# Kernel optimization log

Hardware: AMD Instinct MI355X
Metric: run time of the kernel (lower is better)

The kernel has to match this reference:

```python
import jax, jax.numpy as jnp
from jax import lax
import numpy as np

B = 4096          # batch
EMBED = 32        # embed_dim
HEADS = 2
MEM_SIZE = 4096
MEM_DIM = 256
TOPK = 10
LN_EPS = 1e-5


def setup_inputs() -> dict:
    key = jax.random.key(0)
    ks = jax.random.split(key, 32)
    rn = lambda i, shape, s=0.05: (jax.random.normal(ks[i], shape) * s).astype(jnp.float32)
    return {
        'x': jax.random.normal(ks[0], (B, 1, 28, 28), dtype=jnp.float32),
        'patch_w': rn(1, (32, 1, 4, 4)), 'patch_b': rn(2, (32,)),
        'blk_ln1_g': jnp.ones((2, 32), jnp.float32), 'blk_ln1_b': jnp.zeros((2, 32), jnp.float32),
        'blk_inproj_w': rn(3, (2, 96, 32)), 'blk_inproj_b': rn(4, (2, 96)),
        'blk_outproj_w': rn(5, (2, 32, 32)), 'blk_outproj_b': rn(6, (2, 32)),
        'blk_ln2_g': jnp.ones((2, 32), jnp.float32), 'blk_ln2_b': jnp.zeros((2, 32), jnp.float32),
        'blk_ff1_w': rn(7, (2, 128, 32)), 'blk_ff1_b': rn(8, (2, 128)),
        'blk_ff2_w': rn(9, (2, 32, 128)), 'blk_ff2_b': rn(10, (2, 32)),
        'lat_w': rn(11, (256, 1568)), 'lat_b': rn(12, (256,)),
        'memory': jax.random.normal(ks[13], (MEM_SIZE, MEM_DIM), dtype=jnp.float32),
        'dec_w': rn(14, (3136, 256)), 'dec_b': rn(15, (3136,)),
        'upt1_w': rn(16, (64, 32, 4, 4)), 'upt1_b': rn(17, (32,)),
        'c1_w': rn(18, (32, 32, 3, 3)), 'c1_b': rn(19, (32,)),
        'upt2_w': rn(20, (32, 16, 4, 4)), 'upt2_b': rn(21, (16,)),
        'c2_w': rn(22, (8, 16, 3, 3)), 'c2_b': rn(23, (8,)),
        'c3_w': rn(24, (1, 8, 1, 1)), 'c3_b': rn(25, (1,)),
    }


def _ln(x, g, b):
    m = jnp.mean(x, -1, keepdims=True)
    v = jnp.mean((x - m) ** 2, -1, keepdims=True)
    return (x - m) / jnp.sqrt(v + LN_EPS) * g + b


def _conv2d(x, w, b, stride=1, pad=0):
    out = lax.conv_general_dilated(x, w, (stride, stride), ((pad, pad), (pad, pad)),
                                   dimension_numbers=('NCHW', 'OIHW', 'NCHW'))
    return out + b[None, :, None, None]


def _conv_transpose2d(x, w, b, stride, pad):
    # w in torch layout [in, out, kh, kw]; equivalent fractionally-strided conv
    w_f = jnp.flip(w, (2, 3)).transpose(1, 0, 2, 3)  # OIHW
    k = w.shape[2]
    p = k - 1 - pad
    out = lax.conv_general_dilated(x, w_f, (1, 1), ((p, p), (p, p)),
                                   lhs_dilation=(stride, stride),
                                   dimension_numbers=('NCHW', 'OIHW', 'NCHW'))
    return out + b[None, :, None, None]


def _mha(x, wi, bi, wo, bo):
    Bn, S, D = x.shape
    Dh = D // HEADS
    qkv = x @ wi.T + bi                                  # [B,S,3D]
    q, k, v = jnp.split(qkv, 3, axis=-1)
    sp = lambda t: t.reshape(Bn, S, HEADS, Dh).transpose(0, 2, 1, 3)
    q, k, v = sp(q), sp(k), sp(v)
    scores = jnp.einsum('bhqd,bhkd->bhqk', q, k) / jnp.sqrt(jnp.asarray(Dh, x.dtype))
    att = jax.nn.softmax(scores, axis=-1)
    o = jnp.einsum('bhqk,bhkd->bhqd', att, v).transpose(0, 2, 1, 3).reshape(Bn, S, D)
    return o @ wo.T + bo


def _memory_read(latent, memory):
    # cosine-sim topk softmax-weighted gather (F.normalize eps=1e-12)
    mn = memory / jnp.clip(jnp.linalg.norm(memory, axis=1, keepdims=True), 1e-12)
    xn = latent / jnp.clip(jnp.linalg.norm(latent, axis=1, keepdims=True), 1e-12)
    sim = xn @ mn.T                                       # [B, MEM_SIZE]
    topk_sim, topk_idx = lax.top_k(sim, TOPK)
    w = jax.nn.softmax(topk_sim, axis=1)                  # [B, TOPK]
    sel = memory[topk_idx]                                # [B, TOPK, MEM_DIM]
    return jnp.einsum('bk,bkd->bd', w, sel)


def _forward(x, patch_w, patch_b, blk_ln1_g, blk_ln1_b, blk_inproj_w, blk_inproj_b,
             blk_outproj_w, blk_outproj_b, blk_ln2_g, blk_ln2_b, blk_ff1_w, blk_ff1_b,
             blk_ff2_w, blk_ff2_b, lat_w, lat_b, memory, dec_w, dec_b,
             upt1_w, upt1_b, c1_w, c1_b, upt2_w, upt2_b, c2_w, c2_b, c3_w, c3_b):
    Bn = x.shape[0]
    h = _conv2d(x, patch_w, patch_b, stride=4)            # [B,32,7,7]
    t = h.reshape(Bn, EMBED, 49).transpose(0, 2, 1)       # [B,49,32]
    for i in range(2):                                    # two SwinBlocks
        t = t + _mha(_ln(t, blk_ln1_g[i], blk_ln1_b[i]),
                     blk_inproj_w[i], blk_inproj_b[i], blk_outproj_w[i], blk_outproj_b[i])
        f = _ln(t, blk_ln2_g[i], blk_ln2_b[i])
        f = jax.nn.gelu(f @ blk_ff1_w[i].T + blk_ff1_b[i], approximate=False)
        t = t + (f @ blk_ff2_w[i].T + blk_ff2_b[i])
    latent = t.reshape(Bn, -1) @ lat_w.T + lat_b          # [B,256]
    mem_latent = _memory_read(latent, memory)             # [B,256]
    d = (mem_latent @ dec_w.T + dec_b).reshape(Bn, 64, 7, 7)  # dropout=eval identity
    d = jax.nn.relu(_conv_transpose2d(d, upt1_w, upt1_b, 2, 1))   # [B,32,14,14]
    d = jax.nn.relu(_conv2d(d, c1_w, c1_b, 1, 1))
    d = jax.nn.relu(_conv_transpose2d(d, upt2_w, upt2_b, 2, 1))   # [B,16,28,28]
    d = jax.nn.relu(_conv2d(d, c2_w, c2_b, 1, 1))                 # [B,8,28,28]
    return _conv2d(d, c3_w, c3_b, 1, 0)                           # [B,1,28,28]


def reference(x, patch_w, patch_b, blk_ln1_g, blk_ln1_b, blk_inproj_w, blk_inproj_b,
              blk_outproj_w, blk_outproj_b, blk_ln2_g, blk_ln2_b, blk_ff1_w, blk_ff1_b,
              blk_ff2_w, blk_ff2_b, lat_w, lat_b, memory, dec_w, dec_b,
              upt1_w, upt1_b, c1_w, c1_b, upt2_w, upt2_b, c2_w, c2_b, c3_w, c3_b):
    return _forward(x, patch_w, patch_b, blk_ln1_g, blk_ln1_b, blk_inproj_w, blk_inproj_b,
                    blk_outproj_w, blk_outproj_b, blk_ln2_g, blk_ln2_b, blk_ff1_w, blk_ff1_b,
                    blk_ff2_w, blk_ff2_b, lat_w, lat_b, memory, dec_w, dec_b,
                    upt1_w, upt1_b, c1_w, c1_b, upt2_w, upt2_b, c2_w, c2_b, c3_w, c3_b)
```

## Files before the change

### kernel.cpp

```cpp
#include <hip/hip_runtime.h>
#include <math.h>

#define B_TOT 4096
#define CHUNK 4096

typedef _Float16 half_t;
typedef _Float16 h2 __attribute__((ext_vector_type(2)));
typedef _Float16 h8v __attribute__((ext_vector_type(8)));
typedef float f4v __attribute__((ext_vector_type(4)));
typedef float f2v __attribute__((ext_vector_type(2)));

#if __has_builtin(__builtin_amdgcn_fdot2)
#define FDOT2(a, b, c) __builtin_amdgcn_fdot2((a), (b), (c), false)
#else
#define FDOT2(a, b, c) fmaf((float)(a)[1], (float)(b)[1], fmaf((float)(a)[0], (float)(b)[0], (c)))
#endif

#define KSTR 36
#define VSTR 34
#define KBYTES (49 * 72)
#define WAVE_LDS (49 * 72 + 49 * 136)
#define WI_OFF  (4 * WAVE_LDS)
#define BLOCK_LDS (WI_OFF + 12288)

__global__ __launch_bounds__(256) void k_tokens(
    const float* __restrict__ x, const float* __restrict__ pw, const float* __restrict__ pb,
    const float* __restrict__ ln1g, const float* __restrict__ ln1b,
    const float* __restrict__ wi, const float* __restrict__ bi,
    const float* __restrict__ wo, const float* __restrict__ bo,
    const float* __restrict__ ln2g, const float* __restrict__ ln2b,
    const float* __restrict__ w1, const float* __restrict__ fb1,
    const float* __restrict__ w2t, const float* __restrict__ fb2,
    float* __restrict__ tokens)
{
    __shared__ __align__(16) unsigned char Lraw[BLOCK_LDS];
    const int tid = threadIdx.x;
    const int wv = tid >> 6, lane = tid & 63;
    const int b = blockIdx.x * 4 + wv;
    half_t* Kb = (half_t*)(Lraw + wv * WAVE_LDS);
    float*  Vb = (float*)(Lraw + wv * WAVE_LDS + KBYTES);
    const float* wiL = (const float*)(Lraw + WI_OFF);
    float* Lf = (float*)Lraw;
    const bool is_tok = lane < 49;
    const int s = is_tok ? lane : 48;
    const int py = s / 7, px = s % 7;

    {
        const float4* srcw = (const float4*)(wi);
        float4* dstw = (float4*)(Lraw + WI_OFF);
        for (int e = tid; e < 768; e += 256) dstw[e] = srcw[e];
    }

    f2v xv2[8];
    const float* xb = x + (size_t)b * 784 + py * 112 + px * 4;
    #pragma unroll
    for (int r = 0; r < 4; ++r) {
        float4 vq = *(const float4*)(xb + r * 28);
        f2v lo; lo[0] = vq.x; lo[1] = vq.y;
        f2v hi; hi[0] = vq.z; hi[1] = vq.w;
        xv2[2 * r] = lo; xv2[2 * r + 1] = hi;
    }
    f2v t2[16];
    #pragma unroll
    for (int c = 0; c < 32; ++c) {
        const float* wr = pw + c * 16;
        f2v a2 = (f2v){0.f, 0.f};
        #pragma unroll
        for (int c2 = 0; c2 < 4; ++c2) {
            float4 wq = *(const float4*)&wr[4 * c2];
            f2v w0; w0[0] = wq.x; w0[1] = wq.y;
            f2v w1v; w1v[0] = wq.z; w1v[1] = wq.w;
            a2 += xv2[2 * c2] * w0;
            a2 += xv2[2 * c2 + 1] * w1v;
        }
        t2[c >> 1][c & 1] = pb[c] + a2[0] + a2[1];
    }

    for (int blk = 0; blk < 2; ++blk) {
        const float* bib = bi + blk * 96;

        f2v mu2 = (f2v){0.f, 0.f};
        #pragma unroll
        for (int i = 0; i < 16; ++i) mu2 += t2[i];
        float mu = (mu2[0] + mu2[1]) * 0.03125f;
        f2v mub; mub[0] = mu; mub[1] = mu;
        f2v var2 = (f2v){0.f, 0.f};
        #pragma unroll
        for (int i = 0; i < 16; ++i) { f2v d = t2[i] - mub; var2 += d * d; }
        float rstd = rsqrtf((var2[0] + var2[1]) * 0.03125f + 1e-5f);
        f2v rstd2; rstd2[0] = rstd; rstd2[1] = rstd;
        f2v xn2[16];
        {
            const f2v* g2 = (const f2v*)(ln1g + blk * 32);
            const f2v* bl2 = (const f2v*)(ln1b + blk * 32);
            #pragma unroll
            for (int i = 0; i < 16; ++i)
                xn2[i] = (t2[i] - mub) * rstd2 * g2[i] + bl2[i];
        }

        __syncthreads();

        #pragma unroll 4
        for (int d = 0; d < 32; ++d) {
            const float* wr = wiL + (32 + d) * 32;
            f2v a2 = (f2v){0.f, 0.f};
            #pragma unroll
            for (int c2 = 0; c2 < 8; ++c2) {
                float4 wq = *(const float4*)&wr[4 * c2];
                f2v w0; w0[0] = wq.x; w0[1] = wq.y;
                f2v w1v; w1v[0] = wq.z; w1v[1] = wq.w;
                a2 += xn2[2 * c2] * w0;
                a2 += xn2[2 * c2 + 1] * w1v;
            }
            if (is_tok) Kb[s * KSTR + d] = (half_t)(bib[32 + d] + a2[0] + a2[1]);
        }
        #pragma unroll 4
        for (int d = 0; d < 32; ++d) {
            const float* wr = wiL + (64 + d) * 32;
            f2v a2 = (f2v){0.f, 0.f};
            #pragma unroll
            for (int c2 = 0; c2 < 8; ++c2) {
                float4 wq = *(const float4*)&wr[4 * c2];
                f2v w0; w0[0] = wq.x; w0[1] = wq.y;
                f2v w1v; w1v[0] = wq.z; w1v[1] = wq.w;
                a2 += xn2[2 * c2] * w0;
                a2 += xn2[2 * c2 + 1] * w1v;
            }
            if (is_tok) Vb[s * VSTR + d] = bib[64 + d] + a2[0] + a2[1];
        }
        float q0[32];
        #pragma unroll 4
        for (int d = 0; d < 32; ++d) {
            const float* wr = wiL + d * 32;
            f2v a2 = (f2v){0.f, 0.f};
            #pragma unroll
            for (int c2 = 0; c2 < 8; ++c2) {
                float4 wq = *(const float4*)&wr[4 * c2];
                f2v w0; w0[0] = wq.x; w0[1] = wq.y;
                f2v w1v; w1v[0] = wq.z; w1v[1] = wq.w;
                a2 += xn2[2 * c2] * w0;
                a2 += xn2[2 * c2 + 1] * w1v;
            }
            q0[d] = (bib[d] + a2[0] + a2[1]) * 0.25f;
        }
        h2 qh[16];
        #pragma unroll
        for (int i = 0; i < 16; ++i) {
            h2 hh; hh[0] = (half_t)q0[2 * i]; hh[1] = (half_t)q0[2 * i + 1];
            qh[i] = hh;
        }

        __asm__ volatile("s_waitcnt lgkmcnt(0)" ::: "memory");

        f2v o2[16];
        #pragma unroll
        for (int i = 0; i < 16; ++i) o2[i] = (f2v){0.f, 0.f};
        float l0 = 0.f, l1 = 0.f;
        union H4 { double qd; h2 p[2]; };
        for (int j = 0; j < 49; ++j) {
            const double* kr = (const double*)(Kb + j * KSTR);
            const float* vr = Vb + j * VSTR;
            H4 u0, u1, u2, u3, w0, w1h, w2h, w3;
            u0.qd = kr[0]; u1.qd = kr[1]; u2.qd = kr[2]; u3.qd = kr[3];
            w0.qd = kr[4]; w1h.qd = kr[5]; w2h.qd = kr[6]; w3.qd = kr[7];
            float s0a = 0.f, s0b = 0.f, s1a = 0.f, s1b = 0.f;
            s0a = FDOT2(u0.p[0], qh[0], s0a); s0a = FDOT2(u0.p[1], qh[1], s0a);
            s0b = FDOT2(u1.p[0], qh[2], s0b); s0b = FDOT2(u1.p[1], qh[3], s0b);
            s0a = FDOT2(u2.p[0], qh[4], s0a); s0a = FDOT2(u2.p[1], qh[5], s0a);
            s0b = FDOT2(u3.p[0], qh[6], s0b); s0b = FDOT2(u3.p[1], qh[7], s0b);
            s1a = FDOT2(w0.p[0], qh[8], s1a); s1a = FDOT2(w0.p[1], qh[9], s1a);
            s1b = FDOT2(w1h.p[0], qh[10], s1b); s1b = FDOT2(w1h.p[1], qh[11], s1b);
            s1a = FDOT2(w2h.p[0], qh[12], s1a); s1a = FDOT2(w2h.p[1], qh[13], s1a);
            s1b = FDOT2(w3.p[0], qh[14], s1b); s1b = FDOT2(w3.p[1], qh[15], s1b);
            float p0 = __expf(s0a + s0b), p1 = __expf(s1a + s1b);
            l0 += p0; l1 += p1;
            f2v p02; p02[0] = p0; p02[1] = p0;
            f2v p12; p12[0] = p1; p12[1] = p1;
            #pragma unroll
            for (int i = 0; i < 8; ++i) {
                f2v va = *(const f2v*)&vr[2 * i];
                o2[i] += p02 * va;
                f2v vc = *(const f2v*)&vr[16 + 2 * i];
                o2[8 + i] += p12 * vc;
            }
        }
        {
            float il0 = 1.f / l0, il1 = 1.f / l1;
            f2v il02; il02[0] = il0; il02[1] = il0;
            f2v il12; il12[0] = il1; il12[1] = il1;
            #pragma unroll
            for (int i = 0; i < 8; ++i) { o2[i] *= il02; o2[8 + i] *= il12; }
        }

        #pragma unroll
        for (int c = 0; c < 32; ++c) {
            const float* wr = wo + blk * 1024 + c * 32;
            f2v a2 = (f2v){0.f, 0.f};
            #pragma unroll
            for (int c2 = 0; c2 < 8; ++c2) {
                float4 wq = *(const float4*)&wr[4 * c2];
                f2v w0; w0[0] = wq.x; w0[1] = wq.y;
                f2v w1v; w1v[0] = wq.z; w1v[1] = wq.w;
                a2 += o2[2 * c2] * w0;
                a2 += o2[2 * c2 + 1] * w1v;
            }
            t2[c >> 1][c & 1] += bo[blk * 32 + c] + a2[0] + a2[1];
        }

        mu2 = (f2v){0.f, 0.f};
        #pragma unroll
        for (int i = 0; i < 16; ++i) mu2 += t2[i];
        mu = (mu2[0] + mu2[1]) * 0.03125f;
        mub[0] = mu; mub[1] = mu;
        var2 = (f2v){0.f, 0.f};
        #pragma unroll
        for (int i = 0; i < 16; ++i) { f2v d = t2[i] - mub; var2 += d * d; }
        rstd = rsqrtf((var2[0] + var2[1]) * 0.03125f + 1e-5f);
        rstd2[0] = rstd; rstd2[1] = rstd;
        {
            const f2v* g2 = (const f2v*)(ln2g + blk * 32);
            const f2v* bl2 = (const f2v*)(ln2b + blk * 32);
            #pragma unroll
            for (int i = 0; i < 16; ++i)
                xn2[i] = (t2[i] - mub) * rstd2 * g2[i] + bl2[i];
        }

        __syncthreads();

        {
            const float4* src1 = (const float4*)(w1 + blk * 4096);
            const float4* src2 = (const float4*)(w2t + blk * 4096);
            float4* dst = (float4*)Lraw;
            for (int e = tid; e < 1024; e += 256) dst[e] = src1[e];
            for (int e = tid; e < 1024; e += 256) dst[1024 + e] = src2[e];
            if (blk == 0) {
                const float4* srcw = (const float4*)(wi + 3072);
                float4* dstw = (float4*)(Lraw + WI_OFF);
                for (int e = tid; e < 768; e += 256) dstw[e] = srcw[e];
            }
        }
        __syncthreads();

        const float* w2L = Lf + 4096;
        #pragma unroll 2
        for (int j = 0; j < 128; ++j) {
            const float* wr = Lf + j * 32;
            f2v h2a = (f2v){0.f, 0.f};
            #pragma unroll
            for (int c2 = 0; c2 < 8; ++c2) {
                float4 wq = *(const float4*)&wr[4 * c2];
                f2v w0; w0[0] = wq.x; w0[1] = wq.y;
                f2v w1v; w1v[0] = wq.z; w1v[1] = wq.w;
                h2a += xn2[2 * c2] * w0;
                h2a += xn2[2 * c2 + 1] * w1v;
            }
            float h = fb1[blk * 128 + j] + h2a[0] + h2a[1];
            h = 0.5f * h * (1.f + erff(h * 0.7071067811865476f));
            f2v hh; hh[0] = h; hh[1] = h;
            const float* w2r = w2L + j * 32;
            #pragma unroll
            for (int c2 = 0; c2 < 8; ++c2) {
                float4 wq = *(const float4*)&w2r[4 * c2];
                f2v w0; w0[0] = wq.x; w0[1] = wq.y;
                f2v w1v; w1v[0] = wq.z; w1v[1] = wq.w;
                t2[2 * c2]     += hh * w0;
                t2[2 * c2 + 1] += hh * w1v;
            }
        }
        {
            const f2v* fb22 = (const f2v*)(fb2 + blk * 32);
            #pragma unroll
            for (int i = 0; i < 16; ++i) t2[i] += fb22[i];
        }
    }

    if (is_tok) {
        float* op = tokens + (size_t)b * 1568 + s * 32;
        #pragma unroll
        for (int i = 0; i < 8; ++i) {
            float4 vv = make_float4(t2[2 * i][0], t2[2 * i][1],
                                    t2[2 * i + 1][0], t2[2 * i + 1][1]);
            *(float4*)&op[4 * i] = vv;
        }
    }
}

__global__ __launch_bounds__(256) void k_sgemm(
    const float* __restrict__ A, const float* __restrict__ Bm,
    const float* __restrict__ bias, float* __restrict__ C,
    int M, int N, int K)
{
    __shared__ __align__(16) half_t Ah[64 * 40];
    __shared__ __align__(16) half_t Al[64 * 40];
    __shared__ __align__(16) half_t Bh[128 * 40];
    __shared__ __align__(16) half_t Bl[128 * 40];
    const int tid = threadIdx.x;
    const int n0 = blockIdx.x * 128, m0 = blockIdx.y * 64;
    const int w = tid >> 6, lane = tid & 63;
    const int wm = (w >> 1) * 32, wn = (w & 1) * 64;
    const int lr = lane & 15, lk = lane >> 4;

    const int ar = tid >> 2, aseg = (tid & 3) * 8;
    const int br = tid >> 1, bseg = (tid & 1) * 16;

    f4v acch[2][4], accm[2][4];
    #pragma unroll
    for (int i = 0; i < 2; ++i)
        #pragma unroll
        for (int j = 0; j < 4; ++j) {
            acch[i][j] = (f4v){0.f, 0.f, 0.f, 0.f};
            accm[i][j] = (f4v){0.f, 0.f, 0.f, 0.f};
        }

    for (int k0 = 0; k0 < K; k0 += 32) {
        {
            const float* ap = A + (size_t)(m0 + ar) * K + k0 + aseg;
            float4 a0 = *(const float4*)ap;
            float4 a1 = *(const float4*)(ap + 4);
            float av[8] = {a0.x, a0.y, a0.z, a0.w, a1.x, a1.y, a1.z, a1.w};
            h8v ah, al;
            #pragma unroll
            for (int i = 0; i < 8; ++i) {
                half_t h = (half_t)av[i];
                ah[i] = h;
                al[i] = (half_t)((av[i] - (float)h) * 2048.0f);
            }
            *(h8v*)&Ah[ar * 40 + aseg] = ah;
            *(h8v*)&Al[ar * 40 + aseg] = al;

            const float* bp = Bm + (size_t)(n0 + br) * K + k0 + bseg;
            float4 b0 = *(const float4*)bp;
            float4 b1 = *(const float4*)(bp + 4);
            float4 b2 = *(const float4*)(bp + 8);
            float4 b3 = *(const float4*)(bp + 12);
            float bv[16] = {b0.x, b0.y, b0.z, b0.w, b1.x, b1.y, b1.z, b1.w,
                            b2.x, b2.y, b2.z, b2.w, b3.x, b3.y, b3.z, b3.w};
            h8v bh0, bh1, bl0, bl1;
            #pragma unroll
            for (int i = 0; i < 8; ++i) {
                half_t h = (half_t)bv[i];
                bh0[i] = h;
                bl0[i] = (half_t)((bv[i] - (float)h) * 2048.0f);
                half_t hq = (half_t)bv[8 + i];
                bh1[i] = hq;
                bl1[i] = (half_t)((bv[8 + i] - (float)hq) * 2048.0f);
            }
            *(h8v*)&Bh[br * 40 + bseg]     = bh0;
            *(h8v*)&Bh[br * 40 + bseg + 8] = bh1;
            *(h8v*)&Bl[br * 40 + bseg]     = bl0;
            *(h8v*)&Bl[br * 40 + bseg + 8] = bl1;
        }
        __syncthreads();
        h8v afh[2], afl[2], bfh[4], bfl[4];
        #pragma unroll
        for (int i = 0; i < 2; ++i) {
            afh[i] = *(const h8v*)&Ah[(wm + i * 16 + lr) * 40 + lk * 8];
            afl[i] = *(const h8v*)&Al[(wm + i * 16 + lr) * 40 + lk * 8];
        }
        #pragma unroll
        for (int j = 0; j < 4; ++j) {
            bfh[j] = *(const h8v*)&Bh[(wn + j * 16 + lr) * 40 + lk * 8];
            bfl[j] = *(const h8v*)&Bl[(wn + j * 16 + lr) * 40 + lk * 8];
        }
        #pragma unroll
        for (int i = 0; i < 2; ++i)
            #pragma unroll
            for (int j = 0; j < 4; ++j) {
                acch[i][j] = __builtin_amdgcn_mfma_f32_16x16x32_f16(afh[i], bfh[j], acch[i][j], 0, 0, 0);
                accm[i][j] = __builtin_amdgcn_mfma_f32_16x16x32_f16(afh[i], bfl[j], accm[i][j], 0, 0, 0);
                accm[i][j] = __builtin_amdgcn_mfma_f32_16x16x32_f16(afl[i], bfh[j], accm[i][j], 0, 0, 0);
            }
        __syncthreads();
    }

    #pragma unroll
    for (int j = 0; j < 4; ++j) {
        int n = n0 + wn + j * 16 + lr;
        float bv = bias ? bias[n] : 0.f;
        #pragma unroll
        for (int i = 0; i < 2; ++i) {
            #pragma unroll
            for (int r = 0; r < 4; ++r) {
                int m = m0 + wm + i * 16 + lk * 4 + r;
                C[(size_t)m * N + n] = acch[i][j][r] + accm[i][j][r] * (1.0f / 2048.0f) + bv;
            }
        }
    }
}

__global__ __launch_bounds__(256) void k_dgemm(
    const float* __restrict__ A, const float* __restrict__ Bm,
    const float* __restrict__ bias, half_t* __restrict__ C,
    int M, int N, int K)
{
    __shared__ __align__(16) half_t As[64 * 40];
    __shared__ __align__(16) half_t Bs[128 * 40];
    const int tid = threadIdx.x;
    const int n0 = blockIdx.x * 128, m0 = blockIdx.y * 64;
    const int w = tid >> 6, lane = tid & 63;
    const int wm = (w >> 1) * 32, wn = (w & 1) * 64;
    const int lr = lane & 15, lk = lane >> 4;

    const int ar = tid >> 2, aseg = (tid & 3) * 8;
    const int br = tid >> 1, bseg = (tid & 1) * 16;

    f4v acc[2][4];
    #pragma unroll
    for (int i = 0; i < 2; ++i)
        #pragma unroll
        for (int j = 0; j < 4; ++j) acc[i][j] = (f4v){0.f, 0.f, 0.f, 0.f};

    for (int k0 = 0; k0 < K; k0 += 32) {
        {
            const float* ap = A + (size_t)(m0 + ar) * K + k0 + aseg;
            float4 a0 = *(const float4*)ap;
            float4 a1 = *(const float4*)(ap + 4);
            h8v ha;
            ha[0] = (half_t)a0.x; ha[1] = (half_t)a0.y;
            ha[2] = (half_t)a0.z; ha[3] = (half_t)a0.w;
            ha[4] = (half_t)a1.x; ha[5] = (half_t)a1.y;
            ha[6] = (half_t)a1.z; ha[7] = (half_t)a1.w;
            *(h8v*)&As[ar * 40 + aseg] = ha;

            const float* bp = Bm + (size_t)(n0 + br) * K + k0 + bseg;
            float4 b0 = *(const float4*)bp;
            float4 b1 = *(const float4*)(bp + 4);
            float4 b2 = *(const float4*)(bp + 8);
            float4 b3 = *(const float4*)(bp + 12);
            h8v hb0, hb1;
            hb0[0] = (half_t)b0.x; hb0[1] = (half_t)b0.y;
            hb0[2] = (half_t)b0.z; hb0[3] = (half_t)b0.w;
            hb0[4] = (half_t)b1.x; hb0[5] = (half_t)b1.y;
            hb0[6] = (half_t)b1.z; hb0[7] = (half_t)b1.w;
            hb1[0] = (half_t)b2.x; hb1[1] = (half_t)b2.y;
            hb1[2] = (half_t)b2.z; hb1[3] = (half_t)b2.w;
            hb1[4] = (half_t)b3.x; hb1[5] = (half_t)b3.y;
            hb1[6] = (half_t)b3.z; hb1[7] = (half_t)b3.w;
            *(h8v*)&Bs[br * 40 + bseg] = hb0;
            *(h8v*)&Bs[br * 40 + bseg + 8] = hb1;
        }
        __syncthreads();
        h8v af[2], bfr[4];
        #pragma unroll
        for (int i = 0; i < 2; ++i)
            af[i] = *(const h8v*)&As[(wm + i * 16 + lr) * 40 + lk * 8];
        #pragma unroll
        for (int j = 0; j < 4; ++j)
            bfr[j] = *(const h8v*)&Bs[(wn + j * 16 + lr) * 40 + lk * 8];
        #pragma unroll
        for (int i = 0; i < 2; ++i)
            #pragma unroll
            for (int j = 0; j < 4; ++j)
                acc[i][j] = __builtin_amdgcn_mfma_f32_16x16x32_f16(af[i], bfr[j], acc[i][j], 0, 0, 0);
        __syncthreads();
    }

    #pragma unroll
    for (int j = 0; j < 4; ++j) {
        int n = n0 + wn + j * 16 + lr;
        float bv = bias[n];
        #pragma unroll
        for (int i = 0; i < 2; ++i) {
            #pragma unroll
            for (int r = 0; r < 4; ++r) {
                int m = m0 + wm + i * 16 + lk * 4 + r;
                C[(size_t)m * N + n] = (half_t)fmaxf(acc[i][j][r] + bv, 0.f);
            }
        }
    }
}

__global__ __launch_bounds__(256) void k_fuse(
    const float* __restrict__ wt1, const float* __restrict__ upt1_b,
    const float* __restrict__ dec_w, const float* __restrict__ dec_b,
    float* __restrict__ Wf, float* __restrict__ bf)
{
    __shared__ float WL[4][64][32];
    const int p = blockIdx.x;
    const int k = threadIdx.x;
    const int y = p / 14, x = p % 14;

    int ky0 = 0, iy0 = 0, ky1 = 0, iy1 = 0, nky = 0;
    for (int ky = 0; ky < 4; ++ky) {
        int iyn = y + 1 - ky;
        if (iyn < 0 || (iyn & 1)) continue;
        int iy = iyn >> 1;
        if (iy > 6) continue;
        if (nky == 0) { ky0 = ky; iy0 = iy; } else { ky1 = ky; iy1 = iy; }
        ++nky;
    }
    int kx0 = 0, ix0 = 0, kx1 = 0, ix1 = 0, nkx = 0;
    for (int kx = 0; kx < 4; ++kx) {
        int ixn = x + 1 - kx;
        if (ixn < 0 || (ixn & 1)) continue;
        int ix = ixn >> 1;
        if (ix > 6) continue;
        if (nkx == 0) { kx0 = kx; ix0 = ix; } else { kx1 = kx; ix1 = ix; }
        ++nkx;
    }
    const int ntap = nky * nkx;

    for (int e = k; e < ntap * 2048; e += 256) {
        int t = e >> 11, c = (e >> 5) & 63, o = e & 31;
        int ti = (nkx == 2) ? (t >> 1) : t;
        int tj = (nkx == 2) ? (t & 1) : 0;
        int ky = ti ? ky1 : ky0;
        int kx = tj ? kx1 : kx0;
        WL[t][c][o] = wt1[((c * 32 + o) * 4 + ky) * 4 + kx];
    }
    __syncthreads();

    float acc[32];
    #pragma unroll
    for (int o = 0; o < 32; ++o) acc[o] = 0.f;
    float bacc = 0.f;

    for (int t = 0; t < ntap; ++t) {
        int ti = (nkx == 2) ? (t >> 1) : t;
        int tj = (nkx == 2) ? (t & 1) : 0;
        int iy = ti ? iy1 : iy0;
        int ix = tj ? ix1 : ix0;
        int rbase = iy * 7 + ix;
        for (int c = 0; c < 64; ++c) {
            int row = c * 49 + rbase;
            float v = dec_w[(size_t)row * 256 + k];
            const float* wr = &WL[t][c][0];
            #pragma unroll
            for (int o8 = 0; o8 < 8; ++o8) {
                float4 wq = *(const float4*)&wr[4 * o8];
                acc[4 * o8 + 0] = fmaf(wq.x, v, acc[4 * o8 + 0]);
                acc[4 * o8 + 1] = fmaf(wq.y, v, acc[4 * o8 + 1]);
                acc[4 * o8 + 2] = fmaf(wq.z, v, acc[4 * o8 + 2]);
                acc[4 * o8 + 3] = fmaf(wq.w, v, acc[4 * o8 + 3]);
            }
            if (k < 32) bacc = fmaf(WL[t][c][k], dec_b[row], bacc);
        }
    }

    #pragma unroll 4
    for (int o = 0; o < 32; ++o)
        Wf[((size_t)(p * 32 + o)) * 256 + k] = acc[o];
    if (k < 32) bf[p * 32 + k] = bacc + upt1_b[k];
}

__global__ __launch_bounds__(256) void k_mnorm(const float* __restrict__ mem, float* __restrict__ inv_norm)
{
    __shared__ float red[256];
    const int row = blockIdx.x, tid = threadIdx.x;
    float v = mem[(size_t)row * 256 + tid];
    red[tid] = v * v;
    __syncthreads();
    for (int s = 128; s > 0; s >>= 1) {
        if (tid < s) red[tid] += red[tid + s];
        __syncthreads();
    }
    if (tid == 0) inv_norm[row] = 1.f / fmaxf(sqrtf(red[0]), 1e-12f);
}

__global__ __launch_bounds__(256) void k_memread(
    const float* __restrict__ latent, const float* __restrict__ dots,
    const float* __restrict__ inv_mn, const float* __restrict__ mem,
    float* __restrict__ out)
{
    __shared__ float red[256];
    __shared__ int   redi[4];
    __shared__ float inv_x_s;
    const int b = blockIdx.x, tid = threadIdx.x;
    const int w = tid >> 6, lane = tid & 63;
    float lx = latent[(size_t)b * 256 + tid];
    red[tid] = lx * lx;
    __syncthreads();
    for (int s = 128; s > 0; s >>= 1) {
        if (tid < s) red[tid] += red[tid + s];
        __syncthreads();
    }
    if (tid == 0) inv_x_s = 1.f / fmaxf(sqrtf(red[0]), 1e-12f);
    __syncthreads();
    const float inv_x = inv_x_s;

    float vals[16];
    for (int j = 0; j < 16; ++j) {
        int m = tid + j * 256;
        vals[j] = dots[(size_t)b * 4096 + m] * inv_mn[m] * inv_x;
    }
    float tv[10]; int ti[10];
    for (int t = 0; t < 10; ++t) {
        float bv = -1e30f; int bidx = 0x7fffffff;
        #pragma unroll
        for (int j = 0; j < 16; ++j) {
            int m = tid + j * 256;
            float v = vals[j];
            if (v > bv || (v == bv && m < bidx)) { bv = v; bidx = m; }
        }
        #pragma unroll
        for (int off = 32; off > 0; off >>= 1) {
            float ov = __shfl_xor(bv, off);
            int   oi = __shfl_xor(bidx, off);
            if (ov > bv || (ov == bv && oi < bidx)) { bv = ov; bidx = oi; }
        }
        if (lane == 0) { red[w] = bv; redi[w] = bidx; }
        __syncthreads();
        float fv = red[0]; int fi = redi[0];
        #pragma unroll
        for (int q = 1; q < 4; ++q) {
            float v2 = red[q]; int i2 = redi[q];
            if (v2 > fv || (v2 == fv && i2 < fi)) { fv = v2; fi = i2; }
        }
        tv[t] = fv; ti[t] = fi;
        if ((fi & 255) == tid) vals[fi >> 8] = -1e30f;
        __syncthreads();
    }
    float wgt[10], wsum = 0.f;
    for (int t = 0; t < 10; ++t) { wgt[t] = expf(tv[t] - tv[0]); wsum += wgt[t]; }
    float inv_ws = 1.f / wsum;
    float acc = 0.f;
    for (int t = 0; t < 10; ++t) acc += (wgt[t] * inv_ws) * mem[(size_t)ti[t] * 256 + tid];
    out[(size_t)b * 256 + tid] = acc;
}

__global__ __launch_bounds__(256) void k_pack(
    const float* __restrict__ wc1, const float* __restrict__ wt2,
    const float* __restrict__ wc2, const float* __restrict__ w2src,
    half_t* __restrict__ pk2h, half_t* __restrict__ pk3h,
    float* __restrict__ pk4, float* __restrict__ pk5)
{
    int i = blockIdx.x * 256 + threadIdx.x;
    if (i < 9216) {
        int ic = i & 31, oc = (i >> 5) & 15, nt = (i >> 9) & 1, t = i >> 10;
        pk2h[i] = (half_t)wc1[((nt * 16 + oc) * 32 + ic) * 9 + t];
    }
    if (i < 8192) {
        int ic = i & 31, oc = (i >> 5) & 15, t = (i >> 9) & 3, q = i >> 11;
        int wy = t >> 1, wx = t & 1, py = q >> 1, px = q & 1;
        int ky = 3 - py - 2 * wy, kx = 3 - px - 2 * wx;
        pk3h[i] = (half_t)wt2[((ic * 16 + oc) * 4 + ky) * 4 + kx];
    }
    if (i < 1152) {
        int o = i & 7, tap = (i >> 3) % 9, c = i / 72;
        pk4[i] = wc2[(o * 16 + c) * 9 + tap];
    }
    if (i < 8192) {
        int c = i & 31, j = (i >> 5) & 127, bq = i >> 12;
        pk5[i] = w2src[bq * 4096 + c * 128 + j];
    }
}

__global__ __launch_bounds__(256) void k_conv1(
    const half_t* __restrict__ in, const half_t* __restrict__ wh,
    const float* __restrict__ bias, half_t* __restrict__ out)
{
    __shared__ __align__(16) half_t P[2 * 16 * 16 * 40];
    const int tid = threadIdx.x;
    const int w = tid >> 6, lane = tid & 63;
    const size_t b0 = (size_t)blockIdx.x * 2;

    for (int e = tid; e < 10240; e += 256) ((unsigned int*)P)[e] = 0u;
    __syncthreads();
    {
        const unsigned int* src = (const unsigned int*)in;
        for (int e = tid; e < 6272; e += 256) {
            int si = e / 3136;
            int rem = e - si * 3136;
            int p = rem >> 4, c2 = rem & 15;
            int y = p / 14, x = p % 14;
            ((unsigned int*)P)[si * 5120 + ((y + 1) * 16 + (x + 1)) * 20 + c2] =
                src[(b0 + si) * 3136 + rem];
        }
    }

    h8v bfr[9][2];
    #pragma unroll
    for (int t = 0; t < 9; ++t)
        #pragma unroll
        for (int nt = 0; nt < 2; ++nt)
            bfr[t][nt] = *(const h8v*)&wh[((size_t)((t * 2 + nt) * 16 + (lane & 15))) * 32 + (lane >> 4) * 8];

    __syncthreads();

    const int kseg = (lane >> 4) * 8;
    const int oc = lane & 15;
    const float bv0 = bias[oc], bv1 = bias[16 + oc];

    for (int job = w; job < 26; job += 4) {
        const int si = job >= 13 ? 1 : 0;
        const int tile = job - si * 13;
        int p = tile * 16 + (lane & 15);
        if (p > 195) p = 195;
        const int y = p / 14, x = p % 14;
        const half_t* Pb = P + si * 10240;

        f4v acc0 = (f4v){0.f, 0.f, 0.f, 0.f};
        f4v acc1 = (f4v){0.f, 0.f, 0.f, 0.f};
        #pragma unroll
        for (int ky = 0; ky < 3; ++ky) {
            #pragma unroll
            for (int kx = 0; kx < 3; ++kx) {
                h8v af = *(const h8v*)&Pb[((y + ky) * 16 + (x + kx)) * 40 + kseg];
                acc0 = __builtin_amdgcn_mfma_f32_16x16x32_f16(af, bfr[ky * 3 + kx][0], acc0, 0, 0, 0);
                acc1 = __builtin_amdgcn_mfma_f32_16x16x32_f16(af, bfr[ky * 3 + kx][1], acc1, 0, 0, 0);
            }
        }

        const int pr0 = tile * 16 + (lane >> 4) * 4;
        half_t* ob = out + (b0 + si) * 6272;
        #pragma unroll
        for (int r = 0; r < 4; ++r) {
            int pp = pr0 + r;
            if (pp < 196) {
                ob[(size_t)pp * 32 + oc]      = (half_t)fmaxf(acc0[r] + bv0, 0.f);
                ob[(size_t)pp * 32 + 16 + oc] = (half_t)fmaxf(acc1[r] + bv1, 0.f);
            }
        }
    }
}

__global__ __launch_bounds__(256) void k_convt23(
    const half_t* __restrict__ in, const half_t* __restrict__ pk3h,
    const float* __restrict__ bt2, const float* __restrict__ pk4,
    const float* __restrict__ b2, const float* __restrict__ w3,
    const float* __restrict__ b3, float* __restrict__ out)
{
    __shared__ __align__(16) unsigned char Lraw[30720];
    half_t* Pin = (half_t*)Lraw;
    float*  P2  = (float*)Lraw;
    const int tid = threadIdx.x;
    const int w = tid >> 6, lane = tid & 63;
    const int b = blockIdx.x;

    for (int e = tid; e < 5120; e += 256) ((unsigned int*)Pin)[e] = 0u;
    __syncthreads();
    {
        const unsigned int* src = (const unsigned int*)in;
        for (int e = tid; e < 3136; e += 256) {
            int p = e >> 4, c2 = e & 15;
            int y = p / 14, x = p % 14;
            ((unsigned int*)Pin)[((y + 1) * 16 + (x + 1)) * 20 + c2] =
                src[(size_t)b * 3136 + e];
        }
    }
    __syncthreads();

    const int oc = lane & 15;
    const int kseg = (lane >> 4) * 8;

    f4v res[13];
    #pragma unroll
    for (int j = 0; j < 13; ++j) {
        const int job = w + 4 * j;
        const int q = job / 13, tile = job - q * 13;
        const int py = q >> 1, px = q & 1;
        int p = tile * 16 + (lane & 15);
        if (p > 195) p = 195;
        const int ty = p / 14, tx = p % 14;
        f4v a = (f4v){0.f, 0.f, 0.f, 0.f};
        #pragma unroll
        for (int t = 0; t < 4; ++t) {
            const int wy = t >> 1, wx = t & 1;
            h8v bf = *(const h8v*)&pk3h[((size_t)((q * 4 + t) * 16 + oc)) * 32 + kseg];
            h8v af = *(const h8v*)&Pin[((ty + py + wy) * 16 + (tx + px + wx)) * 40 + kseg];
            a = __builtin_amdgcn_mfma_f32_16x16x32_f16(af, bf, a, 0, 0, 0);
        }
        res[j] = a;
    }
    __syncthreads();

    const bool active2 = tid < 196;
    int row = active2 ? tid / 7 : 0;
    int tx0b = active2 ? (tid % 7) * 4 : 0;
    const float bco = bt2[oc];

    float acc2[4][8];
    #pragma unroll
    for (int i = 0; i < 4; ++i)
        #pragma unroll
        for (int o = 0; o < 8; ++o) acc2[i][o] = 0.f;

    #pragma unroll
    for (int g = 0; g < 2; ++g) {
        for (int e = tid; e < 7680; e += 256) P2[e] = 0.f;
        __syncthreads();
        if ((oc >> 3) == g) {
            #pragma unroll
            for (int j = 0; j < 13; ++j) {
                const int job = w + 4 * j;
                const int q = job / 13, tile = job - q * 13;
                const int py = q >> 1, px = q & 1;
                const int pr0 = tile * 16 + (lane >> 4) * 4;
                #pragma unroll
                for (int r = 0; r < 4; ++r) {
                    int p = pr0 + r;
                    if (p < 196) {
                        int Y = 2 * (p / 14) + py, X = 2 * (p % 14) + px;
                        P2[((oc & 7) * 30 + Y + 1) * 32 + (X + 1)] = fmaxf(res[j][r] + bco, 0.f);
                    }
                }
            }
        }
        __syncthreads();
        for (int cl = 0; cl < 8; ++cl) {
            const float* Pb = &P2[(cl * 30 + row) * 32 + tx0b];
            const float* wb = pk4 + (size_t)(g * 8 + cl) * 72;
            #pragma unroll
            for (int ky = 0; ky < 3; ++ky) {
                float4 a = *(const float4*)&Pb[ky * 32];
                float4 bq = *(const float4*)&Pb[ky * 32 + 4];
                float rowb[8] = {a.x, a.y, a.z, a.w, bq.x, bq.y, bq.z, bq.w};
                #pragma unroll
                for (int kx = 0; kx < 3; ++kx) {
                    const float* wt = wb + (ky * 3 + kx) * 8;
                    #pragma unroll
                    for (int o = 0; o < 8; ++o) {
                        float wv2 = wt[o];
                        #pragma unroll
                        for (int i = 0; i < 4; ++i)
                            acc2[i][o] = fmaf(rowb[i + kx], wv2, acc2[i][o]);
                    }
                }
            }
        }
        __syncthreads();
    }

    if (active2) {
        const float bias3 = b3[0];
        #pragma unroll
        for (int i = 0; i < 4; ++i) {
            float r = bias3;
            #pragma unroll
            for (int o = 0; o < 8; ++o) r += fmaxf(acc2[i][o] + b2[o], 0.f) * w3[o];
            out[(size_t)b * 784 + row * 28 + tx0b + i] = r;
        }
    }
}

extern "C" void kernel_launch(void* const* d_in, const int* in_sizes, int n_in,
                              void* d_out, int out_size, void* d_ws, size_t ws_size,
                              hipStream_t stream)
{
    const float* x       = (const float*)d_in[0];
    const float* patch_w = (const float*)d_in[1];
    const float* patch_b = (const float*)d_in[2];
    const float* ln1g    = (const float*)d_in[3];
    const float* ln1b    = (const float*)d_in[4];
    const float* wi      = (const float*)d_in[5];
    const float* bi      = (const float*)d_in[6];
    const float* wo      = (const float*)d_in[7];
    const float* bo      = (const float*)d_in[8];
    const float* ln2g    = (const float*)d_in[9];
    const float* ln2b    = (const float*)d_in[10];
    const float* w1      = (const float*)d_in[11];
    const float* b1      = (const float*)d_in[12];
    const float* w2      = (const float*)d_in[13];
    const float* b2      = (const float*)d_in[14];
    const float* lat_w   = (const float*)d_in[15];
    const float* lat_b   = (const float*)d_in[16];
    const float* memory  = (const float*)d_in[17];
    const float* dec_w   = (const float*)d_in[18];
    const float* dec_b   = (const float*)d_in[19];
    const float* upt1_w  = (const float*)d_in[20];
    const float* upt1_b  = (const float*)d_in[21];
    const float* c1_w    = (const float*)d_in[22];
    const float* c1_b    = (const float*)d_in[23];
    const float* upt2_w  = (const float*)d_in[24];
    const float* upt2_b  = (const float*)d_in[25];
    const float* c2_w    = (const float*)d_in[26];
    const float* c2_b    = (const float*)d_in[27];
    const float* c3_w    = (const float*)d_in[28];
    const float* c3_b    = (const float*)d_in[29];
    float* outp = (float*)d_out;

    float* ws = (float*)d_ws;
    size_t off = 0;
    auto alloc = [&](size_t n) { float* p = ws + off; off += (n + 63) & ~(size_t)63; return p; };
    float* tokens     = alloc((size_t)B_TOT * 1568);
    float* latent     = alloc((size_t)B_TOT * 256);
    float* dots       = alloc((size_t)B_TOT * 4096);
    float* mem_latent = alloc((size_t)B_TOT * 256);
    float* inv_mn     = alloc(4096);
    half_t* pk2h      = (half_t*)alloc(4608);
    half_t* pk3h      = (half_t*)alloc(4096);
    float* pk4        = alloc(1152);
    float* pk5        = alloc(8192);
    float* Wf         = alloc((size_t)6272 * 256);
    float* bf         = alloc(6272);
    half_t* d1h       = (half_t*)alloc((size_t)CHUNK * 6272 / 2);
    half_t* d2h       = (half_t*)alloc((size_t)CHUNK * 6272 / 2);
    (void)in_sizes; (void)n_in; (void)out_size; (void)ws_size;

    k_pack<<<36, 256, 0, stream>>>(c1_w, upt2_w, c2_w, w2, pk2h, pk3h, pk4, pk5);
    k_fuse<<<196, 256, 0, stream>>>(upt1_w, upt1_b, dec_w, dec_b, Wf, bf);

    k_tokens<<<B_TOT / 4, 256, 0, stream>>>(x, patch_w, patch_b, ln1g, ln1b, wi, bi,
                                            wo, bo, ln2g, ln2b, w1, b1, pk5, b2, tokens);
    k_sgemm<<<dim3(256 / 128, B_TOT / 64), 256, 0, stream>>>(tokens, lat_w, lat_b, latent,
                                                             B_TOT, 256, 1568);
    k_mnorm<<<4096, 256, 0, stream>>>(memory, inv_mn);
    k_sgemm<<<dim3(4096 / 128, B_TOT / 64), 256, 0, stream>>>(latent, memory, nullptr, dots,
                                                              B_TOT, 4096, 256);
    k_memread<<<B_TOT, 256, 0, stream>>>(latent, dots, inv_mn, memory, mem_latent);

    for (int c = 0; c < B_TOT / CHUNK; ++c) {
        const float* ml = mem_latent + (size_t)c * CHUNK * 256;
        k_dgemm<<<dim3(6272 / 128, CHUNK / 64), 256, 0, stream>>>(ml, Wf, bf, d1h,
                                                                  CHUNK, 6272, 256);
        k_conv1  <<<CHUNK / 2, 256, 0, stream>>>(d1h, pk2h, c1_b, d2h);
        k_convt23<<<CHUNK, 256, 0, stream>>>(d2h, pk3h, upt2_b, pk4, c2_b, c3_w, c3_b,
                                             outp + (size_t)c * CHUNK * 784);
    }
}
```

Measured before the change: 1.065 ms.

## Pre-split GEMM B operands to fp16 hi/lo once and use packed f2v FMAs

```diff
diff --git a/kernel.cpp b/kernel.cpp
--- a/kernel.cpp
+++ b/kernel.cpp
@@ -285,10 +285,28 @@
     }
 }
 
+__global__ __launch_bounds__(256) void k_split(
+    const float* __restrict__ lat_w, const float* __restrict__ memory,
+    half_t* __restrict__ lwh, half_t* __restrict__ lwl,
+    half_t* __restrict__ memh, half_t* __restrict__ meml)
+{
+    size_t i = (size_t)blockIdx.x * 256 + threadIdx.x;
+    if (i < 401408) {
+        float v = lat_w[i];
+        half_t h = (half_t)v;
+        lwh[i] = h; lwl[i] = (half_t)((v - (float)h) * 2048.0f);
+    }
+    if (i < 1048576) {
+        float v = memory[i];
+        half_t h = (half_t)v;
+        memh[i] = h; meml[i] = (half_t)((v - (float)h) * 2048.0f);
+    }
+}
+
 __global__ __launch_bounds__(256) void k_sgemm(
-    const float* __restrict__ A, const float* __restrict__ Bm,
-    const float* __restrict__ bias, float* __restrict__ C,
-    int M, int N, int K)
+    const float* __restrict__ A, const half_t* __restrict__ Bhg,
+    const half_t* __restrict__ Blg, const float* __restrict__ bias,
+    float* __restrict__ C, int M, int N, int K)
 {
     __shared__ __align__(16) half_t Ah[64 * 40];
     __shared__ __align__(16) half_t Al[64 * 40];
@@ -328,23 +346,12 @@
             *(h8v*)&Ah[ar * 40 + aseg] = ah;
             *(h8v*)&Al[ar * 40 + aseg] = al;
 
-            const float* bp = Bm + (size_t)(n0 + br) * K + k0 + bseg;
-            float4 b0 = *(const float4*)bp;
-            float4 b1 = *(const float4*)(bp + 4);
-            float4 b2 = *(const float4*)(bp + 8);
-            float4 b3 = *(const float4*)(bp + 12);
-            float bv[16] = {b0.x, b0.y, b0.z, b0.w, b1.x, b1.y, b1.z, b1.w,
-                            b2.x, b2.y, b2.z, b2.w, b3.x, b3.y, b3.z, b3.w};
-            h8v bh0, bh1, bl0, bl1;
-            #pragma unroll
-            for (int i = 0; i < 8; ++i) {
-                half_t h = (half_t)bv[i];
-                bh0[i] = h;
-                bl0[i] = (half_t)((bv[i] - (float)h) * 2048.0f);
-                half_t hq = (half_t)bv[8 + i];
-                bh1[i] = hq;
-                bl1[i] = (half_t)((bv[8 + i] - (float)hq) * 2048.0f);
-            }
+            const half_t* bph = Bhg + (size_t)(n0 + br) * K + k0 + bseg;
+            const half_t* bpl = Blg + (size_t)(n0 + br) * K + k0 + bseg;
+            h8v bh0 = *(const h8v*)bph;
+            h8v bh1 = *(const h8v*)(bph + 8);
+            h8v bl0 = *(const h8v*)bpl;
+            h8v bl1 = *(const h8v*)(bpl + 8);
             *(h8v*)&Bh[br * 40 + bseg]     = bh0;
             *(h8v*)&Bh[br * 40 + bseg + 8] = bh1;
             *(h8v*)&Bl[br * 40 + bseg]     = bl0;
@@ -510,9 +517,9 @@
     }
     __syncthreads();
 
-    float acc[32];
-    #pragma unroll
-    for (int o = 0; o < 32; ++o) acc[o] = 0.f;
+    f2v acc2[16];
+    #pragma unroll
+    for (int o = 0; o < 16; ++o) acc2[o] = (f2v){0.f, 0.f};
     float bacc = 0.f;
 
     for (int t = 0; t < ntap; ++t) {
@@ -524,22 +531,17 @@
         for (int c = 0; c < 64; ++c) {
             int row = c * 49 + rbase;
             float v = dec_w[(size_t)row * 256 + k];
-            const float* wr = &WL[t][c][0];
-            #pragma unroll
-            for (int o8 = 0; o8 < 8; ++o8) {
-                float4 wq = *(const float4*)&wr[4 * o8];
-                acc[4 * o8 + 0] = fmaf(wq.x, v, acc[4 * o8 + 0]);
-                acc[4 * o8 + 1] = fmaf(wq.y, v, acc[4 * o8 + 1]);
-                acc[4 * o8 + 2] = fmaf(wq.z, v, acc[4 * o8 + 2]);
-                acc[4 * o8 + 3] = fmaf(wq.w, v, acc[4 * o8 + 3]);
-            }
+            f2v vv; vv[0] = v; vv[1] = v;
+            const f2v* w2p = (const f2v*)&WL[t][c][0];
+            #pragma unroll
+            for (int o2 = 0; o2 < 16; ++o2) acc2[o2] += vv * w2p[o2];
             if (k < 32) bacc = fmaf(WL[t][c][k], dec_b[row], bacc);
         }
     }
 
     #pragma unroll 4
     for (int o = 0; o < 32; ++o)
-        Wf[((size_t)(p * 32 + o)) * 256 + k] = acc[o];
+        Wf[((size_t)(p * 32 + o)) * 256 + k] = acc2[o >> 1][o & 1];
     if (k < 32) bf[p * 32 + k] = bacc + upt1_b[k];
 }
 
@@ -769,11 +771,11 @@
     int tx0b = active2 ? (tid % 7) * 4 : 0;
     const float bco = bt2[oc];
 
-    float acc2[4][8];
+    f2v acc2[4][4];
     #pragma unroll
     for (int i = 0; i < 4; ++i)
         #pragma unroll
-        for (int o = 0; o < 8; ++o) acc2[i][o] = 0.f;
+        for (int o2 = 0; o2 < 4; ++o2) acc2[i][o2] = (f2v){0.f, 0.f};
 
     #pragma unroll
     for (int g = 0; g < 2; ++g) {
@@ -807,13 +809,14 @@
                 float rowb[8] = {a.x, a.y, a.z, a.w, bq.x, bq.y, bq.z, bq.w};
                 #pragma unroll
                 for (int kx = 0; kx < 3; ++kx) {
-                    const float* wt = wb + (ky * 3 + kx) * 8;
+                    const f2v* wt2p = (const f2v*)(wb + (ky * 3 + kx) * 8);
                     #pragma unroll
-                    for (int o = 0; o < 8; ++o) {
-                        float wv2 = wt[o];
-                        #pragma unroll
-                        for (int i = 0; i < 4; ++i)
-                            acc2[i][o] = fmaf(rowb[i + kx], wv2, acc2[i][o]);
+                    for (int i = 0; i < 4; ++i) {
+                        f2v rb; rb[0] = rowb[i + kx]; rb[1] = rowb[i + kx];
+                        acc2[i][0] += rb * wt2p[0];
+                        acc2[i][1] += rb * wt2p[1];
+                        acc2[i][2] += rb * wt2p[2];
+                        acc2[i][3] += rb * wt2p[3];
                     }
                 }
             }
@@ -827,7 +830,8 @@
         for (int i = 0; i < 4; ++i) {
             float r = bias3;
             #pragma unroll
-            for (int o = 0; o < 8; ++o) r += fmaxf(acc2[i][o] + b2[o], 0.f) * w3[o];
+            for (int o = 0; o < 8; ++o)
+                r += fmaxf(acc2[i][o >> 1][o & 1] + b2[o], 0.f) * w3[o];
             out[(size_t)b * 784 + row * 28 + tx0b + i] = r;
         }
     }
@@ -885,18 +889,23 @@
     float* bf         = alloc(6272);
     half_t* d1h       = (half_t*)alloc((size_t)CHUNK * 6272 / 2);
     half_t* d2h       = (half_t*)alloc((size_t)CHUNK * 6272 / 2);
+    half_t* lwh       = (half_t*)alloc(200704);
+    half_t* lwl       = (half_t*)alloc(200704);
+    half_t* memh      = (half_t*)alloc(524288);
+    half_t* meml      = (half_t*)alloc(524288);
     (void)in_sizes; (void)n_in; (void)out_size; (void)ws_size;
 
     k_pack<<<36, 256, 0, stream>>>(c1_w, upt2_w, c2_w, w2, pk2h, pk3h, pk4, pk5);
+    k_split<<<4096, 256, 0, stream>>>(lat_w, memory, lwh, lwl, memh, meml);
     k_fuse<<<196, 256, 0, stream>>>(upt1_w, upt1_b, dec_w, dec_b, Wf, bf);
 
     k_tokens<<<B_TOT / 4, 256, 0, stream>>>(x, patch_w, patch_b, ln1g, ln1b, wi, bi,
                                             wo, bo, ln2g, ln2b, w1, b1, pk5, b2, tokens);
-    k_sgemm<<<dim3(256 / 128, B_TOT / 64), 256, 0, stream>>>(tokens, lat_w, lat_b, latent,
-                                                             B_TOT, 256, 1568);
+    k_sgemm<<<dim3(256 / 128, B_TOT / 64), 256, 0, stream>>>(tokens, lwh, lwl, lat_b,
+                                                             latent, B_TOT, 256, 1568);
     k_mnorm<<<4096, 256, 0, stream>>>(memory, inv_mn);
-    k_sgemm<<<dim3(4096 / 128, B_TOT / 64), 256, 0, stream>>>(latent, memory, nullptr, dots,
-                                                              B_TOT, 4096, 256);
+    k_sgemm<<<dim3(4096 / 128, B_TOT / 64), 256, 0, stream>>>(latent, memh, meml, nullptr,
+                                                              dots, B_TOT, 4096, 256);
     k_memread<<<B_TOT, 256, 0, stream>>>(latent, dots, inv_mn, memory, mem_latent);
 
     for (int c = 0; c < B_TOT / CHUNK; ++c) {
```

Measured after the change: 1.050 ms. Within noise of the previous version (-1.4%).
